# Optimization experiments

Measured on AMD Instinct MI355X. Metric: run time of the kernel, lower is better.

## Reference

```python
import jax, jax.numpy as jnp
import numpy as np

MIN_MARGIN = 0.15
MAX_MARGIN = 0.6
NUM_CALLS = 1  # first call; margin anneals over 40000 calls in the original
MARGIN = min(MIN_MARGIN + float(NUM_CALLS) / 40000.0 * (MAX_MARGIN - MIN_MARGIN), MAX_MARGIN)

B, C, D = 8192, 20000, 128


def setup_inputs() -> dict:
    key = jax.random.key(0)
    k1, k2, k3 = jax.random.split(key, 3)
    features = jax.random.normal(k1, (B, D), dtype=jnp.float32)
    centers = jax.random.normal(k2, (C, D), dtype=jnp.float32)
    labels = jax.random.randint(k3, (B,), 0, C, dtype=jnp.int64)
    return {"features": features, "centers": centers, "labels": labels}


def reference(features, centers, labels):
    # L2-normalize features along dim 1 (F.normalize default, eps=1e-12)
    norm = jnp.linalg.norm(features, axis=1, keepdims=True)
    f = features / jnp.maximum(norm, 1e-12)

    batch_centers = centers[labels]                       # [B, D]
    pos_distances = 1.0 - jnp.sum(f * batch_centers, axis=1)   # [B]
    neg_distances = 1.0 - jnp.einsum('bd,cd->bc', f, centers)  # [B, C]

    losses = MARGIN + pos_distances[:, None] - neg_distances   # [B, C]

    center_ids = jnp.arange(C, dtype=labels.dtype)
    different_class = labels[:, None] != center_ids[None, :]   # [B, C] bool
    valid = (different_class & (losses > 0.0)).astype(jnp.float32)

    num_valid = jnp.sum(valid)
    total = jnp.sum(losses * valid)
    return jnp.where(num_valid > 0, total / num_valid, jnp.zeros((), dtype=losses.dtype))
```

## Files before the change

kernel.cpp:

```cpp
#include <hip/hip_runtime.h>

#define B_N 8192
#define C_N 20000
#define D_N 128
#define CPAD 20096
#define NTILES32 628
#define NCHUNK 24
#define MARGIN_F 0.15001125f

#define NORM_BLOCKS 2048
#define CONV_BLOCKS 2512

typedef __attribute__((ext_vector_type(8))) short bf16x8;
typedef __attribute__((ext_vector_type(4))) float f32x4;

typedef __attribute__((address_space(1))) const unsigned int GUint;
typedef __attribute__((address_space(3))) unsigned int LUint;

__device__ __forceinline__ unsigned short f2bf(float x) {
    union { float f; unsigned int u; } v; v.f = x;
    unsigned int r = v.u + 0x7fffu + ((v.u >> 16) & 1u);
    return (unsigned short)(r >> 16);
}
__device__ __forceinline__ float bf2f(unsigned short h) {
    union { unsigned int u; float f; } v; v.u = ((unsigned int)h) << 16; return v.f;
}

__global__ __launch_bounds__(256) void k_prep(
    const float* __restrict__ feat, const float* __restrict__ centers,
    const int* __restrict__ labels, unsigned short* __restrict__ fb,
    unsigned short* __restrict__ cb, float* __restrict__ t,
    float* __restrict__ corr_s, unsigned int* __restrict__ corr_c)
{
    const int bid = blockIdx.x;
    if (bid < NORM_BLOCKS) {
        const int lane = threadIdx.x & 63;
        const int row  = bid * 4 + (threadIdx.x >> 6);
        const float2 fv = *(const float2*)(feat + (size_t)row * D_N + lane * 2);
        float ss = fv.x * fv.x + fv.y * fv.y;
        #pragma unroll
        for (int off = 32; off; off >>= 1) ss += __shfl_xor(ss, off);
        const float scale = 1.0f / fmaxf(sqrtf(ss), 1e-12f);
        const float a = fv.x * scale, b = fv.y * scale;
        ushort2 o; o.x = f2bf(a); o.y = f2bf(b);
        *(ushort2*)(fb + (size_t)row * D_N + lane * 2) = o;

        const int lab = labels[row];
        const float2 cv = *(const float2*)(centers + (size_t)lab * D_N + lane * 2);
        float pd = a * cv.x + b * cv.y;
        float pb = bf2f(o.x) * bf2f(f2bf(cv.x)) + bf2f(o.y) * bf2f(f2bf(cv.y));
        #pragma unroll
        for (int off = 32; off; off >>= 1) {
            pd += __shfl_xor(pd, off);
            pb += __shfl_xor(pb, off);
        }
        if (lane == 0) {
            const float tb = MARGIN_F - pd;
            t[row] = tb;
            float cs = fmaxf(tb + pb, 0.0f);
            unsigned int cc = (tb + pb > 0.0f) ? 1u : 0u;
            if (tb > 0.0f) { cs += 96.0f * tb; cc += 96u; }
            corr_s[row] = cs;
            corr_c[row] = cc;
        }
    } else {
        const int idx = (bid - NORM_BLOCKS) * 256 + threadIdx.x;
        const int e = idx * 4;
        const int row = e >> 7;
        ushort4 o;
        if (row < C_N) {
            const float4 v = *(const float4*)(centers + e);
            o.x = f2bf(v.x); o.y = f2bf(v.y); o.z = f2bf(v.z); o.w = f2bf(v.w);
        } else {
            o.x = 0; o.y = 0; o.z = 0; o.w = 0;
        }
        *(ushort4*)(cb + e) = o;
    }
}

__global__ __launch_bounds__(256, 3) void k_main(
    const unsigned short* __restrict__ fb,
    const unsigned short* __restrict__ cb,
    const float* __restrict__ t,
    float* __restrict__ acc_slots)
{
    __shared__ __align__(16) unsigned short sB[2][32 * 128];
    __shared__ float sWsum[4];
    __shared__ unsigned int sWcnt[4];

    const int tid  = threadIdx.x;
    const int lane = tid & 63;
    const int w    = tid >> 6;
    const int chunk   = blockIdx.x;
    const int rowbase = blockIdx.y * 256;
    const int nt = (NTILES32 - 1 - chunk) / NCHUNK + 1;

    const int wf = w * 64;
    const int l15 = lane & 15;
    const int kg  = lane >> 4;

    bf16x8 ffr[4][4];
    float tvr[4];
    #pragma unroll
    for (int ff = 0; ff < 4; ++ff) {
        const int m = rowbase + wf + ff * 16 + l15;
        const unsigned short* src = fb + (size_t)m * D_N + kg * 8;
        #pragma unroll
        for (int ks = 0; ks < 4; ++ks)
            ffr[ks][ff] = *(const bf16x8*)(src + ks * 32);
        tvr[ff] = t[m];
    }

    const char* gB0 = (const char*)cb;
    auto STAGE = [&](int buf, int tile) {
        const char* gB = gB0 + (size_t)tile * 8192;
        #pragma unroll
        for (int i = 0; i < 2; ++i) {
            const int loff = w * 1024 + i * 4096;
            const int x = loff + lane * 16;
            const int sx = x ^ (((x >> 8) & 7) << 4);
            __builtin_amdgcn_global_load_lds((GUint*)(gB + sx),
                (LUint*)((char*)sB[buf] + loff), 16, 0, 0);
        }
    };

    STAGE(0, chunk);
    __syncthreads();

    float ls0 = 0.0f, ls1 = 0.0f;
    unsigned int wcnt = 0;

    for (int j = 0; j < nt; ++j) {
        const int cur = j & 1;
        if (j + 1 < nt) STAGE(cur ^ 1, chunk + (j + 1) * NCHUNK);

        f32x4 acc[2][4];
        #pragma unroll
        for (int fc = 0; fc < 2; ++fc)
            #pragma unroll
            for (int ff = 0; ff < 4; ++ff)
                #pragma unroll
                for (int r = 0; r < 4; ++r)
                    acc[fc][ff][r] = tvr[ff];

        const char* sbase = (const char*)sB[cur];
        #pragma unroll
        for (int ks = 0; ks < 4; ++ks) {
            bf16x8 cfr[2];
            #pragma unroll
            for (int fc = 0; fc < 2; ++fc) {
                const int row = fc * 16 + l15;
                int p = row * 256 + ks * 64 + kg * 16;
                p ^= ((row & 7) << 4);
                cfr[fc] = *(const bf16x8*)(sbase + p);
            }
            #pragma unroll
            for (int fc = 0; fc < 2; ++fc)
                #pragma unroll
                for (int ff = 0; ff < 4; ++ff)
                    acc[fc][ff] = __builtin_amdgcn_mfma_f32_16x16x32_bf16(
                        cfr[fc], ffr[ks][ff], acc[fc][ff], 0, 0, 0);
        }

        #pragma unroll
        for (int fc = 0; fc < 2; ++fc)
            #pragma unroll
            for (int ff = 0; ff < 4; ++ff)
                #pragma unroll
                for (int r = 0; r < 4; ++r) {
                    const float l = acc[fc][ff][r];
                    if (fc == 0) ls0 += fmaxf(l, 0.0f); else ls1 += fmaxf(l, 0.0f);
                    wcnt += (unsigned int)__popcll(__ballot(l > 0.0f));
                }

        __syncthreads();
    }

    float lsum = ls0 + ls1;
    #pragma unroll
    for (int off = 32; off; off >>= 1) lsum += __shfl_xor(lsum, off);
    if (lane == 0) { sWsum[w] = lsum; sWcnt[w] = wcnt; }
    __syncthreads();
    if (tid == 0) {
        float s = 0.0f; unsigned int c = 0;
        #pragma unroll
        for (int i = 0; i < 4; ++i) { s += sWsum[i]; c += sWcnt[i]; }
        const int slot = (blockIdx.x ^ blockIdx.y) & 3;
        atomicAdd(acc_slots + slot * 16, s);
        atomicAdd((unsigned int*)(acc_slots + slot * 16 + 1), c);
    }
}

__global__ __launch_bounds__(256) void k_finalize(
    const float* __restrict__ acc_slots,
    const float* __restrict__ corr_s, const unsigned int* __restrict__ corr_c,
    float* __restrict__ out)
{
    __shared__ float ss[4];
    __shared__ unsigned int sc[4];
    const int tid = threadIdx.x;
    const int lane = tid & 63;
    const int w = tid >> 6;
    float cs = 0.0f; unsigned int cc = 0;
    for (int i = tid; i < B_N; i += 256) { cs += corr_s[i]; cc += corr_c[i]; }
    #pragma unroll
    for (int off = 32; off; off >>= 1) {
        cs += __shfl_xor(cs, off);
        cc += __shfl_xor(cc, off);
    }
    if (lane == 0) { ss[w] = cs; sc[w] = cc; }
    __syncthreads();
    if (tid == 0) {
        float S = -(ss[0] + ss[1] + ss[2] + ss[3]);
        long long C = -(long long)(sc[0] + sc[1] + sc[2] + sc[3]);
        #pragma unroll
        for (int i = 0; i < 4; ++i) {
            S += acc_slots[i * 16];
            C += (long long)((const unsigned int*)acc_slots)[i * 16 + 1];
        }
        out[0] = (C > 0) ? (S / (float)C) : 0.0f;
    }
}

extern "C" void kernel_launch(void* const* d_in, const int* in_sizes, int n_in,
                              void* d_out, int out_size, void* d_ws, size_t ws_size,
                              hipStream_t stream) {
    const float* feat    = (const float*)d_in[0];
    const float* centers = (const float*)d_in[1];
    const int*   labels  = (const int*)d_in[2];
    float* out = (float*)d_out;

    char* ws = (char*)d_ws;
    float*          acc_slots = (float*)ws;
    float*          t         = (float*)(ws + 1024);
    float*          corr_s    = (float*)(ws + 65536);
    unsigned int*   corr_c    = (unsigned int*)(ws + 98304);
    unsigned short* fb        = (unsigned short*)(ws + 131072);
    unsigned short* cb        = (unsigned short*)(ws + 4*1024*1024);

    hipMemsetAsync(ws, 0, 256, stream);
    k_prep<<<NORM_BLOCKS + CONV_BLOCKS, 256, 0, stream>>>(
        feat, centers, labels, fb, cb, t, corr_s, corr_c);
    dim3 grid(NCHUNK, 32);
    k_main<<<grid, 256, 0, stream>>>(fb, cb, t, acc_slots);
    k_finalize<<<1, 256, 0, stream>>>(acc_slots, corr_s, corr_c, out);
}
```

Baseline: 74.02 us.

## Triple-buffer center tiles with explicit vmcnt waits and raw barriers

Replaces the double-buffered LDS staging of center tiles with a three-deep ring. Each iteration now waits with a partial s_waitcnt vmcnt and a raw s_barrier instead of a full __syncthreads. The refill of a buffer is issued right after its MFMA compute and before the ReLU/ballot epilogue, so global-to-LDS loads overlap more of the work. MFMA sections are also given higher wave priority via s_setprio. This uses more LDS, which may limit occupancy, and relies on hand-counted vmcnt values being correct.

```diff
diff --git a/kernel.cpp b/kernel.cpp
--- a/kernel.cpp
+++ b/kernel.cpp
@@ -84,7 +84,7 @@
     const float* __restrict__ t,
     float* __restrict__ acc_slots)
 {
-    __shared__ __align__(16) unsigned short sB[2][32 * 128];
+    __shared__ __align__(16) unsigned short sB[3][32 * 128];
     __shared__ float sWsum[4];
     __shared__ unsigned int sWcnt[4];
 
@@ -125,16 +125,15 @@
     };
 
     STAGE(0, chunk);
-    __syncthreads();
+    STAGE(1, chunk + NCHUNK);
+    STAGE(2, chunk + 2 * NCHUNK);
 
     float ls0 = 0.0f, ls1 = 0.0f;
     unsigned int wcnt = 0;
 
-    for (int j = 0; j < nt; ++j) {
-        const int cur = j & 1;
-        if (j + 1 < nt) STAGE(cur ^ 1, chunk + (j + 1) * NCHUNK);
-
-        f32x4 acc[2][4];
+    f32x4 acc[2][4];
+
+    auto COMPUTE = [&](int cur) {
         #pragma unroll
         for (int fc = 0; fc < 2; ++fc)
             #pragma unroll
@@ -144,6 +143,7 @@
                     acc[fc][ff][r] = tvr[ff];
 
         const char* sbase = (const char*)sB[cur];
+        __builtin_amdgcn_s_setprio(1);
         #pragma unroll
         for (int ks = 0; ks < 4; ++ks) {
             bf16x8 cfr[2];
@@ -161,7 +161,10 @@
                     acc[fc][ff] = __builtin_amdgcn_mfma_f32_16x16x32_bf16(
                         cfr[fc], ffr[ks][ff], acc[fc][ff], 0, 0, 0);
         }
-
+        __builtin_amdgcn_s_setprio(0);
+    };
+
+    auto EPILOGUE = [&]() {
         #pragma unroll
         for (int fc = 0; fc < 2; ++fc)
             #pragma unroll
@@ -172,9 +175,33 @@
                     if (fc == 0) ls0 += fmaxf(l, 0.0f); else ls1 += fmaxf(l, 0.0f);
                     wcnt += (unsigned int)__popcll(__ballot(l > 0.0f));
                 }
-
-        __syncthreads();
-    }
+    };
+
+#define SBAR() do {                                       \
+        __builtin_amdgcn_sched_barrier(0);                \
+        __builtin_amdgcn_s_barrier();                     \
+        __builtin_amdgcn_sched_barrier(0);                \
+    } while (0)
+
+    for (int j = 0; j < nt - 2; ++j) {
+        asm volatile("s_waitcnt vmcnt(4)" ::: "memory");
+        SBAR();
+        COMPUTE(j % 3);
+        SBAR();
+        if (j + 3 < nt) STAGE(j % 3, chunk + (j + 3) * NCHUNK);
+        EPILOGUE();
+    }
+    {
+        asm volatile("s_waitcnt vmcnt(2)" ::: "memory");
+        SBAR();
+        COMPUTE((nt - 2) % 3);
+        EPILOGUE();
+        asm volatile("s_waitcnt vmcnt(0)" ::: "memory");
+        SBAR();
+        COMPUTE((nt - 1) % 3);
+        EPILOGUE();
+    }
+#undef SBAR
 
     float lsum = ls0 + ls1;
     #pragma unroll
```

After: 74.17 us. No clear change (+0.2%).

## Give each wave private LDS tiles of 16 centers and drop block barriers

Applied to the files above, without the earlier changes.

Each wave now stages its own 16-row center tile into a private double buffer in LDS, replacing the shared 32-row tile that all four waves read. Loads are issued two tiles ahead and ordered with explicit vmcnt/lgkmcnt waits instead of __syncthreads, so waves no longer stall on each other. Chunk count rises to 32 and occupancy is targeted at 4 blocks per CU. In exchange, each wave fetches the same center tiles separately, so global and LDS traffic per block rises about fourfold and reuse across waves is lost. The hand-written waitcnt values must exactly match how many loads are in flight.

```diff
diff --git a/kernel.cpp b/kernel.cpp
--- a/kernel.cpp
+++ b/kernel.cpp
@@ -4,8 +4,8 @@
 #define C_N 20000
 #define D_N 128
 #define CPAD 20096
-#define NTILES32 628
-#define NCHUNK 24
+#define NTILES16 1256
+#define NCHUNK 32
 #define MARGIN_F 0.15001125f
 
 #define NORM_BLOCKS 2048
@@ -78,13 +78,13 @@
     }
 }
 
-__global__ __launch_bounds__(256, 3) void k_main(
+__global__ __launch_bounds__(256, 4) void k_main(
     const unsigned short* __restrict__ fb,
     const unsigned short* __restrict__ cb,
     const float* __restrict__ t,
     float* __restrict__ acc_slots)
 {
-    __shared__ __align__(16) unsigned short sB[2][32 * 128];
+    __shared__ __align__(16) char sB[4 * 2 * 4096];
     __shared__ float sWsum[4];
     __shared__ unsigned int sWcnt[4];
 
@@ -93,7 +93,7 @@
     const int w    = tid >> 6;
     const int chunk   = blockIdx.x;
     const int rowbase = blockIdx.y * 256;
-    const int nt = (NTILES32 - 1 - chunk) / NCHUNK + 1;
+    const int nt = (NTILES16 - 1 - chunk) / NCHUNK + 1;
 
     const int wf = w * 64;
     const int l15 = lane & 15;
@@ -111,69 +111,62 @@
         tvr[ff] = t[m];
     }
 
-    const char* gB0 = (const char*)cb;
     auto STAGE = [&](int buf, int tile) {
-        const char* gB = gB0 + (size_t)tile * 8192;
-        #pragma unroll
-        for (int i = 0; i < 2; ++i) {
-            const int loff = w * 1024 + i * 4096;
-            const int x = loff + lane * 16;
+        const char* g = (const char*)cb + (size_t)tile * 4096;
+        #pragma unroll
+        for (int i = 0; i < 4; ++i) {
+            const int loff = w * 8192 + buf * 4096 + i * 1024;
+            const int x = i * 1024 + lane * 16;
             const int sx = x ^ (((x >> 8) & 7) << 4);
-            __builtin_amdgcn_global_load_lds((GUint*)(gB + sx),
-                (LUint*)((char*)sB[buf] + loff), 16, 0, 0);
+            __builtin_amdgcn_global_load_lds((GUint*)(g + sx),
+                (LUint*)(sB + loff), 16, 0, 0);
         }
     };
 
     STAGE(0, chunk);
-    __syncthreads();
+    if (nt > 1) STAGE(1, chunk + NCHUNK);
 
     float ls0 = 0.0f, ls1 = 0.0f;
     unsigned int wcnt = 0;
 
     for (int j = 0; j < nt; ++j) {
-        const int cur = j & 1;
-        if (j + 1 < nt) STAGE(cur ^ 1, chunk + (j + 1) * NCHUNK);
-
-        f32x4 acc[2][4];
-        #pragma unroll
-        for (int fc = 0; fc < 2; ++fc)
+        if (j + 1 < nt) { asm volatile("s_waitcnt vmcnt(4)" ::: "memory"); }
+        else            { asm volatile("s_waitcnt vmcnt(0)" ::: "memory"); }
+
+        const char* sbase = sB + w * 8192 + (j & 1) * 4096;
+        bf16x8 cfr[4];
+        #pragma unroll
+        for (int ks = 0; ks < 4; ++ks) {
+            int p = l15 * 256 + ks * 64 + kg * 16;
+            p ^= ((l15 & 7) << 4);
+            cfr[ks] = *(const bf16x8*)(sbase + p);
+        }
+        asm volatile("s_waitcnt lgkmcnt(0)" ::: "memory");
+        __builtin_amdgcn_sched_barrier(0);
+        if (j + 2 < nt) STAGE(j & 1, chunk + (j + 2) * NCHUNK);
+
+        f32x4 acc[4];
+        #pragma unroll
+        for (int ff = 0; ff < 4; ++ff)
+            #pragma unroll
+            for (int r = 0; r < 4; ++r)
+                acc[ff][r] = tvr[ff];
+
+        #pragma unroll
+        for (int ks = 0; ks < 4; ++ks)
             #pragma unroll
             for (int ff = 0; ff < 4; ++ff)
-                #pragma unroll
-                for (int r = 0; r < 4; ++r)
-                    acc[fc][ff][r] = tvr[ff];
-
-        const char* sbase = (const char*)sB[cur];
-        #pragma unroll
-        for (int ks = 0; ks < 4; ++ks) {
-            bf16x8 cfr[2];
+                acc[ff] = __builtin_amdgcn_mfma_f32_16x16x32_bf16(
+                    cfr[ks], ffr[ks][ff], acc[ff], 0, 0, 0);
+
+        #pragma unroll
+        for (int ff = 0; ff < 4; ++ff)
             #pragma unroll
-            for (int fc = 0; fc < 2; ++fc) {
-                const int row = fc * 16 + l15;
-                int p = row * 256 + ks * 64 + kg * 16;
-                p ^= ((row & 7) << 4);
-                cfr[fc] = *(const bf16x8*)(sbase + p);
+            for (int r = 0; r < 4; ++r) {
+                const float l = acc[ff][r];
+                if (ff & 1) ls1 += fmaxf(l, 0.0f); else ls0 += fmaxf(l, 0.0f);
+                wcnt += (unsigned int)__popcll(__ballot(l > 0.0f));
             }
-            #pragma unroll
-            for (int fc = 0; fc < 2; ++fc)
-                #pragma unroll
-                for (int ff = 0; ff < 4; ++ff)
-                    acc[fc][ff] = __builtin_amdgcn_mfma_f32_16x16x32_bf16(
-                        cfr[fc], ffr[ks][ff], acc[fc][ff], 0, 0, 0);
-        }
-
-        #pragma unroll
-        for (int fc = 0; fc < 2; ++fc)
-            #pragma unroll
-            for (int ff = 0; ff < 4; ++ff)
-                #pragma unroll
-                for (int r = 0; r < 4; ++r) {
-                    const float l = acc[fc][ff][r];
-                    if (fc == 0) ls0 += fmaxf(l, 0.0f); else ls1 += fmaxf(l, 0.0f);
-                    wcnt += (unsigned int)__popcll(__ballot(l > 0.0f));
-                }
-
-        __syncthreads();
     }
 
     float lsum = ls0 + ls1;
```

Result: slower. 77.05 us (+4.1%).

## Start MFMA from zero and fold threshold into max, recovering bias in finalize

Applied to the files above, without the earlier changes.

The main kernel no longer seeds the accumulators with the per-row threshold before each tile. The first k-step takes a zero accumulator, and the epilogue computes max(d, -t) and compares d > -t. The per-row t term (CPAD*sum t) is added back in double precision in finalize. The prep kernel also processes two rows per wavefront with float4 loads, and the partial sums are split across four accumulators. This removes per-tile accumulator initialisation moves but changes the floating-point rounding order.

```diff
diff --git a/kernel.cpp b/kernel.cpp
--- a/kernel.cpp
+++ b/kernel.cpp
@@ -4,11 +4,12 @@
 #define C_N 20000
 #define D_N 128
 #define CPAD 20096
+#define NPAD 96
 #define NTILES32 628
 #define NCHUNK 24
 #define MARGIN_F 0.15001125f
 
-#define NORM_BLOCKS 2048
+#define NORM_BLOCKS 1024
 #define CONV_BLOCKS 2512
 
 typedef __attribute__((ext_vector_type(8))) short bf16x8;
@@ -35,33 +36,33 @@
     const int bid = blockIdx.x;
     if (bid < NORM_BLOCKS) {
         const int lane = threadIdx.x & 63;
-        const int row  = bid * 4 + (threadIdx.x >> 6);
-        const float2 fv = *(const float2*)(feat + (size_t)row * D_N + lane * 2);
-        float ss = fv.x * fv.x + fv.y * fv.y;
-        #pragma unroll
-        for (int off = 32; off; off >>= 1) ss += __shfl_xor(ss, off);
+        const int l32  = lane & 31;
+        const int row  = bid * 8 + ((threadIdx.x >> 6) << 1) + (lane >> 5);
+        const float4 fv = *(const float4*)(feat + (size_t)row * D_N + l32 * 4);
+        float ss = fv.x * fv.x + fv.y * fv.y + fv.z * fv.z + fv.w * fv.w;
+        #pragma unroll
+        for (int off = 16; off; off >>= 1) ss += __shfl_xor(ss, off);
         const float scale = 1.0f / fmaxf(sqrtf(ss), 1e-12f);
-        const float a = fv.x * scale, b = fv.y * scale;
-        ushort2 o; o.x = f2bf(a); o.y = f2bf(b);
-        *(ushort2*)(fb + (size_t)row * D_N + lane * 2) = o;
+        const float a0 = fv.x * scale, a1 = fv.y * scale;
+        const float a2 = fv.z * scale, a3 = fv.w * scale;
+        ushort4 o; o.x = f2bf(a0); o.y = f2bf(a1); o.z = f2bf(a2); o.w = f2bf(a3);
+        *(ushort4*)(fb + (size_t)row * D_N + l32 * 4) = o;
 
         const int lab = labels[row];
-        const float2 cv = *(const float2*)(centers + (size_t)lab * D_N + lane * 2);
-        float pd = a * cv.x + b * cv.y;
-        float pb = bf2f(o.x) * bf2f(f2bf(cv.x)) + bf2f(o.y) * bf2f(f2bf(cv.y));
-        #pragma unroll
-        for (int off = 32; off; off >>= 1) {
+        const float4 cv = *(const float4*)(centers + (size_t)lab * D_N + l32 * 4);
+        float pd = a0 * cv.x + a1 * cv.y + a2 * cv.z + a3 * cv.w;
+        float pb = bf2f(o.x) * bf2f(f2bf(cv.x)) + bf2f(o.y) * bf2f(f2bf(cv.y))
+                 + bf2f(o.z) * bf2f(f2bf(cv.z)) + bf2f(o.w) * bf2f(f2bf(cv.w));
+        #pragma unroll
+        for (int off = 16; off; off >>= 1) {
             pd += __shfl_xor(pd, off);
             pb += __shfl_xor(pb, off);
         }
-        if (lane == 0) {
+        if (l32 == 0) {
             const float tb = MARGIN_F - pd;
             t[row] = tb;
-            float cs = fmaxf(tb + pb, 0.0f);
-            unsigned int cc = (tb + pb > 0.0f) ? 1u : 0u;
-            if (tb > 0.0f) { cs += 96.0f * tb; cc += 96u; }
-            corr_s[row] = cs;
-            corr_c[row] = cc;
+            corr_s[row] = fmaxf(tb + pb, 0.0f) + (float)NPAD * fmaxf(tb, 0.0f);
+            corr_c[row] = ((tb + pb > 0.0f) ? 1u : 0u) + ((tb > 0.0f) ? (unsigned)NPAD : 0u);
         }
     } else {
         const int idx = (bid - NORM_BLOCKS) * 256 + threadIdx.x;
@@ -100,7 +101,7 @@
     const int kg  = lane >> 4;
 
     bf16x8 ffr[4][4];
-    float tvr[4];
+    float ntv[4];
     #pragma unroll
     for (int ff = 0; ff < 4; ++ff) {
         const int m = rowbase + wf + ff * 16 + l15;
@@ -108,8 +109,10 @@
         #pragma unroll
         for (int ks = 0; ks < 4; ++ks)
             ffr[ks][ff] = *(const bf16x8*)(src + ks * 32);
-        tvr[ff] = t[m];
-    }
+        ntv[ff] = -t[m];
+    }
+
+    const f32x4 zero4 = {0.0f, 0.0f, 0.0f, 0.0f};
 
     const char* gB0 = (const char*)cb;
     auto STAGE = [&](int buf, int tile) {
@@ -127,23 +130,15 @@
     STAGE(0, chunk);
     __syncthreads();
 
-    float ls0 = 0.0f, ls1 = 0.0f;
+    float ls[4] = {0.0f, 0.0f, 0.0f, 0.0f};
     unsigned int wcnt = 0;
 
     for (int j = 0; j < nt; ++j) {
         const int cur = j & 1;
         if (j + 1 < nt) STAGE(cur ^ 1, chunk + (j + 1) * NCHUNK);
 
+        const char* sbase = (const char*)sB[cur];
         f32x4 acc[2][4];
-        #pragma unroll
-        for (int fc = 0; fc < 2; ++fc)
-            #pragma unroll
-            for (int ff = 0; ff < 4; ++ff)
-                #pragma unroll
-                for (int r = 0; r < 4; ++r)
-                    acc[fc][ff][r] = tvr[ff];
-
-        const char* sbase = (const char*)sB[cur];
         #pragma unroll
         for (int ks = 0; ks < 4; ++ks) {
             bf16x8 cfr[2];
@@ -154,12 +149,21 @@
                 p ^= ((row & 7) << 4);
                 cfr[fc] = *(const bf16x8*)(sbase + p);
             }
-            #pragma unroll
-            for (int fc = 0; fc < 2; ++fc)
+            if (ks == 0) {
                 #pragma unroll
-                for (int ff = 0; ff < 4; ++ff)
-                    acc[fc][ff] = __builtin_amdgcn_mfma_f32_16x16x32_bf16(
-                        cfr[fc], ffr[ks][ff], acc[fc][ff], 0, 0, 0);
+                for (int fc = 0; fc < 2; ++fc)
+                    #pragma unroll
+                    for (int ff = 0; ff < 4; ++ff)
+                        acc[fc][ff] = __builtin_amdgcn_mfma_f32_16x16x32_bf16(
+                            cfr[fc], ffr[0][ff], zero4, 0, 0, 0);
+            } else {
+                #pragma unroll
+                for (int fc = 0; fc < 2; ++fc)
+                    #pragma unroll
+                    for (int ff = 0; ff < 4; ++ff)
+                        acc[fc][ff] = __builtin_amdgcn_mfma_f32_16x16x32_bf16(
+                            cfr[fc], ffr[ks][ff], acc[fc][ff], 0, 0, 0);
+            }
         }
 
         #pragma unroll
@@ -168,15 +172,15 @@
             for (int ff = 0; ff < 4; ++ff)
                 #pragma unroll
                 for (int r = 0; r < 4; ++r) {
-                    const float l = acc[fc][ff][r];
-                    if (fc == 0) ls0 += fmaxf(l, 0.0f); else ls1 += fmaxf(l, 0.0f);
-                    wcnt += (unsigned int)__popcll(__ballot(l > 0.0f));
+                    const float d = acc[fc][ff][r];
+                    ls[fc * 2 + (ff & 1)] += fmaxf(d, ntv[ff]);
+                    wcnt += (unsigned int)__popcll(__ballot(d > ntv[ff]));
                 }
 
         __syncthreads();
     }
 
-    float lsum = ls0 + ls1;
+    float lsum = (ls[0] + ls[1]) + (ls[2] + ls[3]);
     #pragma unroll
     for (int off = 32; off; off >>= 1) lsum += __shfl_xor(lsum, off);
     if (lane == 0) { sWsum[w] = lsum; sWcnt[w] = wcnt; }
@@ -192,33 +196,40 @@
 }
 
 __global__ __launch_bounds__(256) void k_finalize(
-    const float* __restrict__ acc_slots,
+    const float* __restrict__ acc_slots, const float* __restrict__ t,
     const float* __restrict__ corr_s, const unsigned int* __restrict__ corr_c,
     float* __restrict__ out)
 {
-    __shared__ float ss[4];
+    __shared__ float ss[4], st[4];
     __shared__ unsigned int sc[4];
     const int tid = threadIdx.x;
     const int lane = tid & 63;
     const int w = tid >> 6;
-    float cs = 0.0f; unsigned int cc = 0;
-    for (int i = tid; i < B_N; i += 256) { cs += corr_s[i]; cc += corr_c[i]; }
+    float cs = 0.0f, ct = 0.0f; unsigned int cc = 0;
+    for (int i = tid; i < B_N; i += 256) {
+        cs += corr_s[i]; ct += t[i]; cc += corr_c[i];
+    }
     #pragma unroll
     for (int off = 32; off; off >>= 1) {
         cs += __shfl_xor(cs, off);
+        ct += __shfl_xor(ct, off);
         cc += __shfl_xor(cc, off);
     }
-    if (lane == 0) { ss[w] = cs; sc[w] = cc; }
+    if (lane == 0) { ss[w] = cs; st[w] = ct; sc[w] = cc; }
     __syncthreads();
     if (tid == 0) {
-        float S = -(ss[0] + ss[1] + ss[2] + ss[3]);
-        long long C = -(long long)(sc[0] + sc[1] + sc[2] + sc[3]);
+        const double CS = (double)ss[0] + ss[1] + ss[2] + ss[3];
+        const double CT = (double)st[0] + st[1] + st[2] + st[3];
+        const long long CC = (long long)sc[0] + sc[1] + sc[2] + sc[3];
+        double M = 0.0; long long Call = 0;
         #pragma unroll
         for (int i = 0; i < 4; ++i) {
-            S += acc_slots[i * 16];
-            C += (long long)((const unsigned int*)acc_slots)[i * 16 + 1];
-        }
-        out[0] = (C > 0) ? (S / (float)C) : 0.0f;
+            M += (double)acc_slots[i * 16];
+            Call += (long long)((const unsigned int*)acc_slots)[i * 16 + 1];
+        }
+        const double S = M + (double)CPAD * CT - CS;
+        const long long C = Call - CC;
+        out[0] = (C > 0) ? (float)(S / (double)C) : 0.0f;
     }
 }
 
@@ -243,5 +254,5 @@
         feat, centers, labels, fb, cb, t, corr_s, corr_c);
     dim3 grid(NCHUNK, 32);
     k_main<<<grid, 256, 0, stream>>>(fb, cb, t, acc_slots);
-    k_finalize<<<1, 256, 0, stream>>>(acc_slots, corr_s, corr_c, out);
-}
+    k_finalize<<<1, 256, 0, stream>>>(acc_slots, t, corr_s, corr_c, out);
+}
```

Measured after the change: 76.89 us. 1.04x slower.
